# Optimization experiments

Measured on AMD Instinct MI355X. Metric: run time of the kernel, lower is better.

Reference implementation:

```python
import jax, jax.numpy as jnp
import numpy as np

N_NODES = 100000
N_EDGES = 1000000
VOCAB = 128
EMB = 64
HID = 64
N_CLASSES = 2
N_GRAPHS = 2048


def setup_inputs() -> dict:
    key = jax.random.key(0)
    ks = jax.random.split(key, 12)
    x = jax.random.randint(ks[0], (N_NODES,), 0, VOCAB)
    edge_index = jax.random.randint(ks[1], (2, N_EDGES), 0, N_NODES)
    batch = jnp.sort(jax.random.randint(ks[2], (N_NODES,), 0, N_GRAPHS))

    def glorot(k, shape):
        fan = shape[0]
        return jax.random.normal(k, shape, dtype=jnp.float32) / np.sqrt(fan).astype(np.float32)

    emb = jax.random.normal(ks[3], (VOCAB, EMB), dtype=jnp.float32)
    W1_l = glorot(ks[4], (EMB, HID)); b1 = jnp.zeros((HID,), jnp.float32)
    W1_r = glorot(ks[5], (EMB, HID))
    W2_l = glorot(ks[6], (HID, HID)); b2 = jnp.zeros((HID,), jnp.float32)
    W2_r = glorot(ks[7], (HID, HID))
    W_out = glorot(ks[8], (HID, N_CLASSES)); b_out = jnp.zeros((N_CLASSES,), jnp.float32)
    return {"x": x, "edge_index": edge_index, "batch": batch, "emb": emb,
            "W1_l": W1_l, "b1": b1, "W1_r": W1_r,
            "W2_l": W2_l, "b2": b2, "W2_r": W2_r,
            "W_out": W_out, "b_out": b_out}


def _sage_conv(h, src, dst, Wl, bl, Wr):
    # PyG SAGEConv: out = lin_l(mean_{j in N(i)} h_j) + lin_r(h_i); lin_r has no bias
    msgs = h[src]                                                        # [E, D] gather
    agg = jax.ops.segment_sum(msgs, dst, num_segments=N_NODES)          # [N, D] scatter-add
    cnt = jax.ops.segment_sum(jnp.ones((src.shape[0], 1), h.dtype), dst,
                              num_segments=N_NODES)                      # [N, 1] degree
    mean = agg / jnp.maximum(cnt, 1.0)
    return mean @ Wl + bl + h @ Wr


def reference(x, edge_index, batch, emb, W1_l, b1, W1_r, W2_l, b2, W2_r, W_out, b_out):
    src, dst = edge_index[0], edge_index[1]
    h = emb[x]                                                           # [N, EMB]
    h = jax.nn.relu(_sage_conv(h, src, dst, W1_l, b1, W1_r))             # [N, HID]
    h = jax.nn.relu(_sage_conv(h, src, dst, W2_l, b2, W2_r))             # [N, HID]
    # global_mean_pool over graph ids
    gsum = jax.ops.segment_sum(h, batch, num_segments=N_GRAPHS)          # [G, HID]
    gcnt = jax.ops.segment_sum(jnp.ones((N_NODES, 1), h.dtype), batch,
                               num_segments=N_GRAPHS)
    pooled = gsum / jnp.maximum(gcnt, 1.0)
    return pooled @ W_out + b_out                                        # [G, C]
```

## Files before the change

kernel.cpp:

```cpp
#include <hip/hip_runtime.h>
#include <hip/hip_bf16.h>

#define N_NODES 100000
#define N_EDGES 1000000
#define EMB 64
#define HID 64
#define VOCAB 128
#define N_GRAPHS 2048

#define CBUCKET 256
#define NBK ((N_NODES + CBUCKET - 1) / CBUCKET)
#define CAP 4096
#define CHUNK 2048
#define SCAT_BLOCKS ((N_EDGES + CHUNK - 1) / CHUNK)
#define GB ((N_NODES + 255) / 256)
#define NPAD 100128
#define OVF_CAP 65536
#define ZROW 0x1FFFF

#define BCASTF(v, l) __int_as_float(__builtin_amdgcn_readlane(__float_as_int(v), (l)))

typedef __attribute__((ext_vector_type(8))) short short8;
typedef __attribute__((ext_vector_type(4))) float f32x4;
typedef __attribute__((ext_vector_type(2))) float f32x2;

__device__ __forceinline__ float bf2f(unsigned short u) {
    return __uint_as_float((unsigned)u << 16);
}
__device__ __forceinline__ float bf2f_lo(unsigned u) {
    return __uint_as_float(u << 16);
}
__device__ __forceinline__ float bf2f_hi(unsigned u) {
    return __uint_as_float(u & 0xffff0000u);
}
__device__ __forceinline__ unsigned short f2bf(float f) {
    return __bfloat16_as_ushort(__float2bfloat16(f));
}

__global__ __launch_bounds__(256) void scatter_kernel(
    const int* __restrict__ src, const int* __restrict__ dst,
    const int* __restrict__ x,
    int* __restrict__ cursor, unsigned* __restrict__ edge8,
    const int* __restrict__ batch, int* __restrict__ gstart,
    const float* __restrict__ emb, const float* __restrict__ W1l,
    const float* __restrict__ W1r,
    const float* __restrict__ W2l, const float* __restrict__ W2r,
    unsigned short* __restrict__ w1frag, unsigned short* __restrict__ w2frag,
    unsigned char* __restrict__ p8z)
{
    __shared__ unsigned earr[CHUNK];
    __shared__ unsigned short karr[CHUNK];
    __shared__ int bcnt[NBK];
    __shared__ int bbase[NBK];
    int b = blockIdx.x;
    int t = threadIdx.x;

    if (b < SCAT_BLOCKS) {
        for (int i = t; i < NBK; i += 256) bcnt[i] = 0;
        __syncthreads();
        int e0 = b * CHUNK;
        int n = min(e0 + CHUNK, N_EDGES) - e0;
        for (int i = t; i < n; i += 256) {
            int d = dst[e0 + i];
            int s = src[e0 + i];
            int xv = x[s];
            int k = d >> 8;
            earr[i] = (unsigned)s | ((unsigned)xv << 17) | ((unsigned)(d & 255) << 24);
            karr[i] = (unsigned short)k;
            atomicAdd(&bcnt[k], 1);
        }
        __syncthreads();
        for (int i = t; i < NBK; i += 256) {
            int c = bcnt[i];
            bbase[i] = i * CAP + (c ? atomicAdd(&cursor[i], c) : 0);
            bcnt[i] = 0;
        }
        __syncthreads();
        for (int i = t; i < n; i += 256) {
            int k = karr[i];
            int off = atomicAdd(&bcnt[k], 1);
            edge8[bbase[k] + off] = earr[i];
        }
    } else if (b < SCAT_BLOCKS + GB) {
        int i = (b - SCAT_BLOCKS) * 256 + t;
        if (i >= N_NODES) return;
        int bg = batch[i];
        int bp = (i == 0) ? -1 : batch[i - 1];
        for (int g = bp + 1; g <= bg; ++g) gstart[g] = i;
        if (i == N_NODES - 1)
            for (int g = bg + 1; g <= N_GRAPHS; ++g) gstart[g] = N_NODES;
    } else {
        int vb = b - SCAT_BLOCKS - GB;
        if (vb == 0 && t < 16)
            ((unsigned*)(p8z + (size_t)ZROW * 64))[t] = 0u;

        int wave = t >> 6, lane = t & 63;
        int v = vb * 4 + wave;
        {
            float er = emb[v * 64 + lane];
            float al = 0.f, ar = 0.f;
#pragma unroll 8
            for (int d = 0; d < 64; ++d) {
                float e = BCASTF(er, d);
                al += e * W1l[d * 64 + lane];
                ar += e * W1r[d * 64 + lane];
            }
            int reml = (v >> 3) & 3, jj = v & 7;
            int ll = (reml << 4) | (lane & 15);
            int nt = lane >> 4;
            int gl = ((((v >> 5)) * 4 + nt) * 64 + ll) * 8 + jj;
            int gr = ((((v >> 5) + 4) * 4 + nt) * 64 + ll) * 8 + jj;
            w1frag[gl] = f2bf(al);
            w1frag[gr] = f2bf(ar);
        }
        int g = vb * 256 + t;
        int j = g & 7, l = (g >> 3) & 63, h = (g >> 9) & 1, tt = g >> 10;
        int k = h * 32 + ((l >> 4) * 8) + j;
        int n = tt * 16 + (l & 15);
        float w = (n < 64) ? W2l[k * 64 + n] : W2r[k * 64 + (n - 64)];
        w2frag[g] = f2bf(w);
    }
}

__global__ __launch_bounds__(256) void sage1_kernel(
    const int* __restrict__ x,
    const unsigned* __restrict__ edge8, const int* __restrict__ cursor,
    int* __restrict__ dcnt, int* __restrict__ col32g,
    int2* __restrict__ ovf, int* __restrict__ ovf_cnt,
    const unsigned short* __restrict__ w1frag,
    const unsigned short* __restrict__ w2frag, const float* __restrict__ b1,
    unsigned char* __restrict__ p8, unsigned short* __restrict__ q16)
{
    __shared__ unsigned hist[128 * 32];
    __shared__ __align__(16) unsigned short msbuf[128 * 72];
    __shared__ int cnt[128];
    __shared__ int xl[128];
    __shared__ float invd[128];
    int* col32l = (int*)msbuf;

    int blk = blockIdx.x, bucket = blk >> 1, half = blk & 1;
    int t = threadIdx.x;
    int nbase = bucket * CBUCKET + half * 128;

    for (int i = t * 4; i < 128 * 32; i += 1024)
        *(uint4*)&hist[i] = (uint4){0u, 0u, 0u, 0u};
    if (t < 128) {
        cnt[t] = 0;
        int node = nbase + t;
        xl[t] = (node < N_NODES) ? x[node] : 0;
    }
    __syncthreads();

    int lo = bucket * CAP, ecnt = cursor[bucket];
    for (int i = t; i < ecnt; i += 256) {
        unsigned e = edge8[lo + i];
        int ld = (int)(e >> 24);
        if ((ld >> 7) == half) {
            int r = ld & 127;
            int slot = atomicAdd(&cnt[r], 1);
            int pay = (int)(e & 0x1FFFF);
            if (slot < 32) {
                col32l[r * 32 + slot] = pay;
            } else {
                int w = atomicAdd(ovf_cnt, 1);
                if (w < OVF_CAP) ovf[w] = make_int2(nbase + r, pay);
            }
            int xv = (int)((e >> 17) & 127);
            int wc = (xv >> 2) ^ ((r & 7) << 2);
            atomicAdd(&hist[r * 32 + wc], 1u << ((xv & 3) * 8));
        }
    }
    __syncthreads();

    {
        int4* dstp = (int4*)&col32g[(size_t)nbase * 32];
        const int4* srcp = (const int4*)col32l;
        for (int j = t; j < 1024; j += 256)
            dstp[j] = srcp[j];
        if (t < 128) {
            dcnt[nbase + t] = cnt[t];
            invd[t] = 1.0f / fmaxf((float)cnt[t], 1.0f);
        }
    }
    __syncthreads();

    int wave = t >> 6, lane = t & 63;
    int m = lane & 15;
    int qd = lane >> 4;
    int hswz = (m & 7) << 2;

#pragma unroll
    for (int rt = wave * 2; rt < wave * 2 + 2; ++rt) {
        short8 acnt[4], aself[4];
#pragma unroll
        for (int kf = 0; kf < 4; ++kf) {
            int w0 = (kf * 8 + qd * 2) ^ hswz;
            uint2 u = *(const uint2*)&hist[(rt * 16 + m) * 32 + w0];
            short8 f;
            f[0] = (short)f2bf((float)(u.x & 255));
            f[1] = (short)f2bf((float)((u.x >> 8) & 255));
            f[2] = (short)f2bf((float)((u.x >> 16) & 255));
            f[3] = (short)f2bf((float)(u.x >> 24));
            f[4] = (short)f2bf((float)(u.y & 255));
            f[5] = (short)f2bf((float)((u.y >> 8) & 255));
            f[6] = (short)f2bf((float)((u.y >> 16) & 255));
            f[7] = (short)f2bf((float)(u.y >> 24));
            acnt[kf] = f;
        }
        int xv = xl[rt * 16 + m];
#pragma unroll
        for (int kf = 0; kf < 4; ++kf) {
            int v = xv - kf * 32 - qd * 8;
            short8 f;
#pragma unroll
            for (int j = 0; j < 8; ++j)
                f[j] = (v == j) ? (short)0x3F80 : (short)0;
            aself[kf] = f;
        }
        float iv0 = invd[rt * 16 + qd * 4 + 0];
        float iv1 = invd[rt * 16 + qd * 4 + 1];
        float iv2 = invd[rt * 16 + qd * 4 + 2];
        float iv3 = invd[rt * 16 + qd * 4 + 3];

#pragma unroll
        for (int nt = 0; nt < 4; ++nt) {
            f32x4 accA = {0.f, 0.f, 0.f, 0.f};
            f32x4 accS = {0.f, 0.f, 0.f, 0.f};
#pragma unroll
            for (int kf = 0; kf < 4; ++kf) {
                short8 bA = *(const short8*)(w1frag + ((kf * 4 + nt) * 64 + lane) * 8);
                accA = __builtin_amdgcn_mfma_f32_16x16x32_bf16(acnt[kf], bA, accA, 0, 0, 0);
            }
#pragma unroll
            for (int kf = 0; kf < 4; ++kf) {
                short8 bS = *(const short8*)(w1frag + (((kf + 4) * 4 + nt) * 64 + lane) * 8);
                accS = __builtin_amdgcn_mfma_f32_16x16x32_bf16(aself[kf], bS, accS, 0, 0, 0);
            }
            int c = nt * 16 + m;
            float b1c = b1[c];
            int rb = rt * 16 + qd * 4;
            msbuf[(rb + 0) * 72 + c] = f2bf(fmaxf(accA[0] * iv0 + accS[0] + b1c, 0.f));
            msbuf[(rb + 1) * 72 + c] = f2bf(fmaxf(accA[1] * iv1 + accS[1] + b1c, 0.f));
            msbuf[(rb + 2) * 72 + c] = f2bf(fmaxf(accA[2] * iv2 + accS[2] + b1c, 0.f));
            msbuf[(rb + 3) * 72 + c] = f2bf(fmaxf(accA[3] * iv3 + accS[3] + b1c, 0.f));
        }
    }
    __syncthreads();

#pragma unroll
    for (int rt = wave * 2; rt < wave * 2 + 2; ++rt) {
        const unsigned short* arow = &msbuf[(rt * 16 + m) * 72 + qd * 8];
        short8 a0 = *(const short8*)(arow);
        short8 a1 = *(const short8*)(arow + 32);
        int rowb = nbase + rt * 16 + qd * 4;

#pragma unroll
        for (int tt = 0; tt < 8; ++tt) {
            short8 b0 = *(const short8*)(w2frag + tt * 1024 + lane * 8);
            short8 b1v = *(const short8*)(w2frag + tt * 1024 + 512 + lane * 8);
            f32x4 acc = {0.f, 0.f, 0.f, 0.f};
            acc = __builtin_amdgcn_mfma_f32_16x16x32_bf16(a0, b0, acc, 0, 0, 0);
            acc = __builtin_amdgcn_mfma_f32_16x16x32_bf16(a1, b1v, acc, 0, 0, 0);
            int o = tt * 16 + m;
            if (o < 64) {
                int pk01 = __builtin_amdgcn_cvt_pk_fp8_f32(acc[0], acc[1], 0, false);
                int pk23 = __builtin_amdgcn_cvt_pk_fp8_f32(acc[2], acc[3], 0, false);
                if (rowb + 0 < N_NODES) p8[(rowb + 0) * 64 + o] = (unsigned char)(pk01 & 0xff);
                if (rowb + 1 < N_NODES) p8[(rowb + 1) * 64 + o] = (unsigned char)((pk01 >> 8) & 0xff);
                if (rowb + 2 < N_NODES) p8[(rowb + 2) * 64 + o] = (unsigned char)(pk23 & 0xff);
                if (rowb + 3 < N_NODES) p8[(rowb + 3) * 64 + o] = (unsigned char)((pk23 >> 8) & 0xff);
            } else {
                int oc = o & 63;
#pragma unroll
                for (int i = 0; i < 4; ++i)
                    if (rowb + i < N_NODES)
                        q16[(rowb + i) * 64 + oc] = f2bf(acc[i]);
            }
        }
    }
}

#define S2_NPW 8
__global__ __launch_bounds__(256) void sage2_kernel(
    const unsigned char* __restrict__ p, const unsigned short* __restrict__ q,
    const int* __restrict__ deg, const int* __restrict__ col32,
    const int2* __restrict__ ovf, const int* __restrict__ ovf_cnt,
    const float* __restrict__ b2,
    const float* __restrict__ Wout, const int* __restrict__ batch,
    float* __restrict__ gsum)
{
    int t = threadIdx.x;
    int wave = t >> 6, lane = t & 63;
    int base_node = (blockIdx.x * 4 + wave) * S2_NPW;
    int c = lane & 15;
    int g = lane >> 4;

    float4 b2v = ((const float4*)b2)[c];
    float4 w01 = ((const float4*)Wout)[c * 2];
    float4 w23 = ((const float4*)Wout)[c * 2 + 1];

    int dgs[S2_NPW];
#pragma unroll
    for (int n = 0; n < S2_NPW; ++n)
        dgs[n] = deg[base_node + n];

#define ACC(a, v) { f32x2 f01_ = __builtin_amdgcn_cvt_pk_f32_fp8((int)(v), false); \
                    f32x2 f23_ = __builtin_amdgcn_cvt_pk_f32_fp8((int)(v), true);  \
                    (a).x += f01_.x; (a).y += f01_.y; (a).z += f23_.x; (a).w += f23_.y; }

#pragma unroll
    for (int hb = 0; hb < 2; ++hb) {
        int nb = hb * 4;

        unsigned vc = (unsigned)((base_node + nb) * 128 + g * 4);
        unsigned i00, i01, i02, i03, i10, i11, i12, i13;
        unsigned i20, i21, i22, i23, i30, i31, i32, i33;
        asm volatile(
            "global_load_dword %0,  %16, %17\n\t"
            "global_load_dword %1,  %16, %17 offset:16\n\t"
            "global_load_dword %2,  %16, %17 offset:32\n\t"
            "global_load_dword %3,  %16, %17 offset:48\n\t"
            "global_load_dword %4,  %16, %17 offset:128\n\t"
            "global_load_dword %5,  %16, %17 offset:144\n\t"
            "global_load_dword %6,  %16, %17 offset:160\n\t"
            "global_load_dword %7,  %16, %17 offset:176\n\t"
            "global_load_dword %8,  %16, %17 offset:256\n\t"
            "global_load_dword %9,  %16, %17 offset:272\n\t"
            "global_load_dword %10, %16, %17 offset:288\n\t"
            "global_load_dword %11, %16, %17 offset:304\n\t"
            "global_load_dword %12, %16, %17 offset:384\n\t"
            "global_load_dword %13, %16, %17 offset:400\n\t"
            "global_load_dword %14, %16, %17 offset:416\n\t"
            "global_load_dword %15, %16, %17 offset:432\n\t"
            "s_waitcnt vmcnt(0)"
            : "=&v"(i00), "=&v"(i01), "=&v"(i02), "=&v"(i03),
              "=&v"(i10), "=&v"(i11), "=&v"(i12), "=&v"(i13),
              "=&v"(i20), "=&v"(i21), "=&v"(i22), "=&v"(i23),
              "=&v"(i30), "=&v"(i31), "=&v"(i32), "=&v"(i33)
            : "v"(vc), "s"(col32)
            : "memory");

        unsigned cc4 = (unsigned)(c << 2);
        int d0 = dgs[nb + 0], d1 = dgs[nb + 1], d2 = dgs[nb + 2], d3 = dgs[nb + 3];
#define SEL(i_, dg_, k_) ((((k_) * 4 + g) < (dg_)) ? ((i_) & 0x1FFFFu) : (unsigned)ZROW)
        unsigned o00 = (SEL(i00, d0, 0) << 6) + cc4, o01 = (SEL(i01, d0, 1) << 6) + cc4;
        unsigned o02 = (SEL(i02, d0, 2) << 6) + cc4, o03 = (SEL(i03, d0, 3) << 6) + cc4;
        unsigned o10 = (SEL(i10, d1, 0) << 6) + cc4, o11 = (SEL(i11, d1, 1) << 6) + cc4;
        unsigned o12 = (SEL(i12, d1, 2) << 6) + cc4, o13 = (SEL(i13, d1, 3) << 6) + cc4;
        unsigned o20 = (SEL(i20, d2, 0) << 6) + cc4, o21 = (SEL(i21, d2, 1) << 6) + cc4;
        unsigned o22 = (SEL(i22, d2, 2) << 6) + cc4, o23 = (SEL(i23, d2, 3) << 6) + cc4;
        unsigned o30 = (SEL(i30, d3, 0) << 6) + cc4, o31 = (SEL(i31, d3, 1) << 6) + cc4;
        unsigned o32 = (SEL(i32, d3, 2) << 6) + cc4, o33 = (SEL(i33, d3, 3) << 6) + cc4;
#undef SEL
        unsigned vq = (unsigned)((base_node + nb) * 128 + c * 8);

        unsigned v00, v01, v02, v03, v10, v11, v12, v13;
        unsigned v20, v21, v22, v23, v30, v31, v32, v33;
        unsigned qa0, qb0, qa1, qb1, qa2, qb2, qa3, qb3;
        asm volatile(
            "global_load_dword %0,  %24, %41\n\t"
            "global_load_dword %1,  %25, %41\n\t"
            "global_load_dword %2,  %26, %41\n\t"
            "global_load_dword %3,  %27, %41\n\t"
            "global_load_dword %4,  %28, %41\n\t"
            "global_load_dword %5,  %29, %41\n\t"
            "global_load_dword %6,  %30, %41\n\t"
            "global_load_dword %7,  %31, %41\n\t"
            "global_load_dword %8,  %32, %41\n\t"
            "global_load_dword %9,  %33, %41\n\t"
            "global_load_dword %10, %34, %41\n\t"
            "global_load_dword %11, %35, %41\n\t"
            "global_load_dword %12, %36, %41\n\t"
            "global_load_dword %13, %37, %41\n\t"
            "global_load_dword %14, %38, %41\n\t"
            "global_load_dword %15, %39, %41\n\t"
            "global_load_dword %16, %40, %42\n\t"
            "global_load_dword %17, %40, %42 offset:4\n\t"
            "global_load_dword %18, %40, %42 offset:128\n\t"
            "global_load_dword %19, %40, %42 offset:132\n\t"
            "global_load_dword %20, %40, %42 offset:256\n\t"
            "global_load_dword %21, %40, %42 offset:260\n\t"
            "global_load_dword %22, %40, %42 offset:384\n\t"
            "global_load_dword %23, %40, %42 offset:388\n\t"
            "s_waitcnt vmcnt(0)"
            : "=&v"(v00), "=&v"(v01), "=&v"(v02), "=&v"(v03),
              "=&v"(v10), "=&v"(v11), "=&v"(v12), "=&v"(v13),
              "=&v"(v20), "=&v"(v21), "=&v"(v22), "=&v"(v23),
              "=&v"(v30), "=&v"(v31), "=&v"(v32), "=&v"(v33),
              "=&v"(qa0), "=&v"(qb0), "=&v"(qa1), "=&v"(qb1),
              "=&v"(qa2), "=&v"(qb2), "=&v"(qa3), "=&v"(qb3)
            : "v"(o00), "v"(o01), "v"(o02), "v"(o03),
              "v"(o10), "v"(o11), "v"(o12), "v"(o13),
              "v"(o20), "v"(o21), "v"(o22), "v"(o23),
              "v"(o30), "v"(o31), "v"(o32), "v"(o33),
              "v"(vq), "s"(p), "s"(q)
            : "memory");

#pragma unroll
        for (int pp = 0; pp < 2; ++pp) {
            int na = nb + pp * 2, nbd = nb + pp * 2 + 1;
            int dgA = dgs[na], dgB = dgs[nbd];
            int nodeA = base_node + na, nodeB = base_node + nbd;

            float4 aA = {0.f,0.f,0.f,0.f}, aB = {0.f,0.f,0.f,0.f};
            if (pp == 0) {
                ACC(aA, v00) ACC(aA, v01) ACC(aA, v02) ACC(aA, v03)
                ACC(aB, v10) ACC(aB, v11) ACC(aB, v12) ACC(aB, v13)
            } else {
                ACC(aA, v20) ACC(aA, v21) ACC(aA, v22) ACC(aA, v23)
                ACC(aB, v30) ACC(aB, v31) ACC(aB, v32) ACC(aB, v33)
            }

            if (dgA > 16) {
                for (int j = 16; j < 32 && j < dgA; j += 8) {
                    int r0 = j + g, r1 = j + 4 + g;
                    unsigned i0 = (r0 < dgA) ? ((unsigned)col32[(size_t)nodeA * 32 + r0] & 0x1FFFFu) : (unsigned)ZROW;
                    unsigned i1 = (r1 < dgA) ? ((unsigned)col32[(size_t)nodeA * 32 + r1] & 0x1FFFFu) : (unsigned)ZROW;
                    unsigned u0 = *(const unsigned*)(p + ((size_t)i0 << 6) + c * 4);
                    unsigned u1 = *(const unsigned*)(p + ((size_t)i1 << 6) + c * 4);
                    ACC(aA, u0) ACC(aA, u1)
                }
                if (dgA > 32) {
                    int ovn = *ovf_cnt; if (ovn > OVF_CAP) ovn = OVF_CAP;
                    for (int k = 0; k < ovn; ++k) {
                        int2 e = ovf[k];
                        if (e.x == nodeA) {
                            unsigned i_ = (unsigned)e.y & 0x1FFFFu;
                            unsigned u = *(const unsigned*)(p + ((size_t)i_ << 6) + c * 4);
                            if (g == 0) ACC(aA, u)
                        }
                    }
                }
            }
            if (dgB > 16) {
                for (int j = 16; j < 32 && j < dgB; j += 8) {
                    int r0 = j + g, r1 = j + 4 + g;
                    unsigned i0 = (r0 < dgB) ? ((unsigned)col32[(size_t)nodeB * 32 + r0] & 0x1FFFFu) : (unsigned)ZROW;
                    unsigned i1 = (r1 < dgB) ? ((unsigned)col32[(size_t)nodeB * 32 + r1] & 0x1FFFFu) : (unsigned)ZROW;
                    unsigned u0 = *(const unsigned*)(p + ((size_t)i0 << 6) + c * 4);
                    unsigned u1 = *(const unsigned*)(p + ((size_t)i1 << 6) + c * 4);
                    ACC(aB, u0) ACC(aB, u1)
                }
                if (dgB > 32) {
                    int ovn = *ovf_cnt; if (ovn > OVF_CAP) ovn = OVF_CAP;
                    for (int k = 0; k < ovn; ++k) {
                        int2 e = ovf[k];
                        if (e.x == nodeB) {
                            unsigned i_ = (unsigned)e.y & 0x1FFFFu;
                            unsigned u = *(const unsigned*)(p + ((size_t)i_ << 6) + c * 4);
                            if (g == 0) ACC(aB, u)
                        }
                    }
                }
            }

            aA.x += __shfl_xor(aA.x, 16, 64); aA.y += __shfl_xor(aA.y, 16, 64);
            aA.z += __shfl_xor(aA.z, 16, 64); aA.w += __shfl_xor(aA.w, 16, 64);
            aB.x += __shfl_xor(aB.x, 16, 64); aB.y += __shfl_xor(aB.y, 16, 64);
            aB.z += __shfl_xor(aB.z, 16, 64); aB.w += __shfl_xor(aB.w, 16, 64);
            aA.x += __shfl_xor(aA.x, 32, 64); aA.y += __shfl_xor(aA.y, 32, 64);
            aA.z += __shfl_xor(aA.z, 32, 64); aA.w += __shfl_xor(aA.w, 32, 64);
            aB.x += __shfl_xor(aB.x, 32, 64); aB.y += __shfl_xor(aB.y, 32, 64);
            aB.z += __shfl_xor(aB.z, 32, 64); aB.w += __shfl_xor(aB.w, 32, 64);

#pragma unroll
            for (int e = 0; e < 2; ++e) {
                int node = base_node + nb + pp * 2 + e;
                int dg = (e == 0) ? dgA : dgB;
                float4 a = (e == 0) ? aA : aB;
                int li = pp * 2 + e;
                unsigned qlo = (li == 0) ? qa0 : (li == 1) ? qa1 : (li == 2) ? qa2 : qa3;
                unsigned qhi = (li == 0) ? qb0 : (li == 1) ? qb1 : (li == 2) ? qb2 : qb3;
                float inv = 1.0f / fmaxf((float)dg, 1.0f);
                float h0 = fmaxf(a.x * inv + b2v.x + bf2f_lo(qlo), 0.f);
                float h1 = fmaxf(a.y * inv + b2v.y + bf2f_hi(qlo), 0.f);
                float h2 = fmaxf(a.z * inv + b2v.z + bf2f_lo(qhi), 0.f);
                float h3 = fmaxf(a.w * inv + b2v.w + bf2f_hi(qhi), 0.f);

                float p0 = h0 * w01.x + h1 * w01.z + h2 * w23.x + h3 * w23.z;
                float p1 = h0 * w01.y + h1 * w01.w + h2 * w23.y + h3 * w23.w;
                if (g != 0) { p0 = 0.f; p1 = 0.f; }
                p0 += __shfl_down(p0, 8, 64);  p1 += __shfl_down(p1, 8, 64);
                p0 += __shfl_down(p0, 4, 64);  p1 += __shfl_down(p1, 4, 64);
                p0 += __shfl_down(p0, 2, 64);  p1 += __shfl_down(p1, 2, 64);
                p0 += __shfl_down(p0, 1, 64);  p1 += __shfl_down(p1, 1, 64);
                if (lane == 0) {
                    int grp = batch[node];
                    atomicAdd(&gsum[grp * 2 + 0], p0);
                    atomicAdd(&gsum[grp * 2 + 1], p1);
                }
            }
        }
    }
#undef ACC
}

__global__ __launch_bounds__(256) void finalize_kernel(
    const float* __restrict__ gsum, const int* __restrict__ gstart,
    const float* __restrict__ bout, float* __restrict__ out)
{
    int g = blockIdx.x * 256 + threadIdx.x;
    if (g >= N_GRAPHS) return;
    int cnt = gstart[g + 1] - gstart[g];
    float inv = 1.0f / fmaxf((float)cnt, 1.0f);
    out[g * 2 + 0] = gsum[g * 2 + 0] * inv + bout[0];
    out[g * 2 + 1] = gsum[g * 2 + 1] * inv + bout[1];
}

extern "C" void kernel_launch(void* const* d_in, const int* in_sizes, int n_in,
                              void* d_out, int out_size, void* d_ws, size_t ws_size,
                              hipStream_t stream) {
    const int*   x    = (const int*)  d_in[0];
    const int*   ei   = (const int*)  d_in[1];
    const int*   batch= (const int*)  d_in[2];
    const float* emb  = (const float*)d_in[3];
    const float* W1l  = (const float*)d_in[4];
    const float* b1   = (const float*)d_in[5];
    const float* W1r  = (const float*)d_in[6];
    const float* W2l  = (const float*)d_in[7];
    const float* b2   = (const float*)d_in[8];
    const float* W2r  = (const float*)d_in[9];
    const float* Wout = (const float*)d_in[10];
    const float* bout = (const float*)d_in[11];
    float* out = (float*)d_out;

    const int* src = ei;
    const int* dst = ei + N_EDGES;

    char* ws = (char*)d_ws;
    size_t off = 0;
    unsigned char*  p8     = (unsigned char*) (ws + off); off += (size_t)(ZROW + 1) * 64;
    unsigned short* q16    = (unsigned short*)(ws + off); off += (size_t)N_NODES * 64 * 2;
    unsigned short* w2frag = (unsigned short*)(ws + off); off += (size_t)8192 * 2;
    unsigned short* w1frag = (unsigned short*)(ws + off); off += (size_t)16384 * 2;
    int*      col32  = (int*)     (ws + off); off += (size_t)NPAD * 32 * 4;
    int2*     ovf    = (int2*)    (ws + off); off += (size_t)OVF_CAP * 8;
    unsigned* edge8  = (unsigned*)(ws + off); off += (size_t)NBK * CAP * 4;
    int*      dcnt   = (int*)     (ws + off); off += (size_t)NPAD * 4;
    int*      gstart = (int*)     (ws + off); off += (size_t)(N_GRAPHS + 2) * 4;
    int*      cursor = (int*)     (ws + off); off += (size_t)NBK * 4;
    int*      ovfcnt = (int*)     (ws + off); off += (size_t)4;
    float*    gsum   = (float*)   (ws + off); off += (size_t)N_GRAPHS * 2 * 4;

    hipMemsetAsync(cursor, 0, (size_t)NBK * 4 + 4 + (size_t)N_GRAPHS * 2 * 4, stream);

    scatter_kernel<<<SCAT_BLOCKS + GB + 32, 256, 0, stream>>>(
        src, dst, x, cursor, edge8,
        batch, gstart, emb, W1l, W1r, W2l, W2r, w1frag, w2frag, p8);
    sage1_kernel<<<NBK * 2, 256, 0, stream>>>(
        x, edge8, cursor, dcnt, col32, ovf, ovfcnt,
        w1frag, w2frag, b1, p8, q16);
    sage2_kernel<<<N_NODES / (4 * S2_NPW), 256, 0, stream>>>(
        p8, q16, dcnt, col32, ovf, ovfcnt, b2, Wout, batch, gsum);
    finalize_kernel<<<(N_GRAPHS + 255) / 256, 256, 0, stream>>>(gsum, gstart, bout, out);
}
```

Baseline: 195.3 us.

## Pad bucket cursors, double scatter chunk, prefill neighbor slots with zero row

Spaces each bucket's cursor counter 64 bytes apart so that atomics on neighbouring buckets no longer contend on the same cache line. The scatter chunk is doubled so fewer blocks issue cursor atomics. The per-node neighbor slot table is prefilled with the zero-row index, which lets the second-layer gather drop its per-slot degree comparisons and masking and run the 16–32 loop at a fixed trip count. In exchange there are some redundant zero-row loads for low-degree nodes, larger per-block shared arrays in scatter, and a larger memset.

```diff
diff --git a/kernel.cpp b/kernel.cpp
--- a/kernel.cpp
+++ b/kernel.cpp
@@ -11,7 +11,7 @@
 #define CBUCKET 256
 #define NBK ((N_NODES + CBUCKET - 1) / CBUCKET)
 #define CAP 4096
-#define CHUNK 2048
+#define CHUNK 4096
 #define SCAT_BLOCKS ((N_EDGES + CHUNK - 1) / CHUNK)
 #define GB ((N_NODES + 255) / 256)
 #define NPAD 100128
@@ -72,7 +72,7 @@
         __syncthreads();
         for (int i = t; i < NBK; i += 256) {
             int c = bcnt[i];
-            bbase[i] = i * CAP + (c ? atomicAdd(&cursor[i], c) : 0);
+            bbase[i] = i * CAP + (c ? atomicAdd(&cursor[i << 4], c) : 0);
             bcnt[i] = 0;
         }
         __syncthreads();
@@ -142,8 +142,10 @@
     int t = threadIdx.x;
     int nbase = bucket * CBUCKET + half * 128;
 
-    for (int i = t * 4; i < 128 * 32; i += 1024)
+    for (int i = t * 4; i < 128 * 32; i += 1024) {
         *(uint4*)&hist[i] = (uint4){0u, 0u, 0u, 0u};
+        *(int4*)&col32l[i] = (int4){ZROW, ZROW, ZROW, ZROW};
+    }
     if (t < 128) {
         cnt[t] = 0;
         int node = nbase + t;
@@ -151,7 +153,7 @@
     }
     __syncthreads();
 
-    int lo = bucket * CAP, ecnt = cursor[bucket];
+    int lo = bucket * CAP, ecnt = cursor[bucket << 4];
     for (int i = t; i < ecnt; i += 256) {
         unsigned e = edge8[lo + i];
         int ld = (int)(e >> 24);
@@ -341,17 +343,14 @@
             : "memory");
 
         unsigned cc4 = (unsigned)(c << 2);
-        int d0 = dgs[nb + 0], d1 = dgs[nb + 1], d2 = dgs[nb + 2], d3 = dgs[nb + 3];
-#define SEL(i_, dg_, k_) ((((k_) * 4 + g) < (dg_)) ? ((i_) & 0x1FFFFu) : (unsigned)ZROW)
-        unsigned o00 = (SEL(i00, d0, 0) << 6) + cc4, o01 = (SEL(i01, d0, 1) << 6) + cc4;
-        unsigned o02 = (SEL(i02, d0, 2) << 6) + cc4, o03 = (SEL(i03, d0, 3) << 6) + cc4;
-        unsigned o10 = (SEL(i10, d1, 0) << 6) + cc4, o11 = (SEL(i11, d1, 1) << 6) + cc4;
-        unsigned o12 = (SEL(i12, d1, 2) << 6) + cc4, o13 = (SEL(i13, d1, 3) << 6) + cc4;
-        unsigned o20 = (SEL(i20, d2, 0) << 6) + cc4, o21 = (SEL(i21, d2, 1) << 6) + cc4;
-        unsigned o22 = (SEL(i22, d2, 2) << 6) + cc4, o23 = (SEL(i23, d2, 3) << 6) + cc4;
-        unsigned o30 = (SEL(i30, d3, 0) << 6) + cc4, o31 = (SEL(i31, d3, 1) << 6) + cc4;
-        unsigned o32 = (SEL(i32, d3, 2) << 6) + cc4, o33 = (SEL(i33, d3, 3) << 6) + cc4;
-#undef SEL
+        unsigned o00 = (i00 << 6) + cc4, o01 = (i01 << 6) + cc4;
+        unsigned o02 = (i02 << 6) + cc4, o03 = (i03 << 6) + cc4;
+        unsigned o10 = (i10 << 6) + cc4, o11 = (i11 << 6) + cc4;
+        unsigned o12 = (i12 << 6) + cc4, o13 = (i13 << 6) + cc4;
+        unsigned o20 = (i20 << 6) + cc4, o21 = (i21 << 6) + cc4;
+        unsigned o22 = (i22 << 6) + cc4, o23 = (i23 << 6) + cc4;
+        unsigned o30 = (i30 << 6) + cc4, o31 = (i31 << 6) + cc4;
+        unsigned o32 = (i32 << 6) + cc4, o33 = (i33 << 6) + cc4;
         unsigned vq = (unsigned)((base_node + nb) * 128 + c * 8);
 
         unsigned v00, v01, v02, v03, v10, v11, v12, v13;
@@ -412,10 +411,9 @@
             }
 
             if (dgA > 16) {
-                for (int j = 16; j < 32 && j < dgA; j += 8) {
-                    int r0 = j + g, r1 = j + 4 + g;
-                    unsigned i0 = (r0 < dgA) ? ((unsigned)col32[(size_t)nodeA * 32 + r0] & 0x1FFFFu) : (unsigned)ZROW;
-                    unsigned i1 = (r1 < dgA) ? ((unsigned)col32[(size_t)nodeA * 32 + r1] & 0x1FFFFu) : (unsigned)ZROW;
+                for (int j = 16; j < 32; j += 8) {
+                    unsigned i0 = (unsigned)col32[(size_t)nodeA * 32 + j + g];
+                    unsigned i1 = (unsigned)col32[(size_t)nodeA * 32 + j + 4 + g];
                     unsigned u0 = *(const unsigned*)(p + ((size_t)i0 << 6) + c * 4);
                     unsigned u1 = *(const unsigned*)(p + ((size_t)i1 << 6) + c * 4);
                     ACC(aA, u0) ACC(aA, u1)
@@ -433,10 +431,9 @@
                 }
             }
             if (dgB > 16) {
-                for (int j = 16; j < 32 && j < dgB; j += 8) {
-                    int r0 = j + g, r1 = j + 4 + g;
-                    unsigned i0 = (r0 < dgB) ? ((unsigned)col32[(size_t)nodeB * 32 + r0] & 0x1FFFFu) : (unsigned)ZROW;
-                    unsigned i1 = (r1 < dgB) ? ((unsigned)col32[(size_t)nodeB * 32 + r1] & 0x1FFFFu) : (unsigned)ZROW;
+                for (int j = 16; j < 32; j += 8) {
+                    unsigned i0 = (unsigned)col32[(size_t)nodeB * 32 + j + g];
+                    unsigned i1 = (unsigned)col32[(size_t)nodeB * 32 + j + 4 + g];
                     unsigned u0 = *(const unsigned*)(p + ((size_t)i0 << 6) + c * 4);
                     unsigned u1 = *(const unsigned*)(p + ((size_t)i1 << 6) + c * 4);
                     ACC(aB, u0) ACC(aB, u1)
@@ -538,11 +535,11 @@
     unsigned* edge8  = (unsigned*)(ws + off); off += (size_t)NBK * CAP * 4;
     int*      dcnt   = (int*)     (ws + off); off += (size_t)NPAD * 4;
     int*      gstart = (int*)     (ws + off); off += (size_t)(N_GRAPHS + 2) * 4;
-    int*      cursor = (int*)     (ws + off); off += (size_t)NBK * 4;
+    int*      cursor = (int*)     (ws + off); off += (size_t)NBK * 16 * 4;
     int*      ovfcnt = (int*)     (ws + off); off += (size_t)4;
     float*    gsum   = (float*)   (ws + off); off += (size_t)N_GRAPHS * 2 * 4;
 
-    hipMemsetAsync(cursor, 0, (size_t)NBK * 4 + 4 + (size_t)N_GRAPHS * 2 * 4, stream);
+    hipMemsetAsync(cursor, 0, (size_t)NBK * 16 * 4 + 4 + (size_t)N_GRAPHS * 2 * 4, stream);
 
     scatter_kernel<<<SCAT_BLOCKS + GB + 32, 256, 0, stream>>>(
         src, dst, x, cursor, edge8,
```

Result: faster. 182.8 us (-6.4%).
